# Kernel optimization log

Measured on AMD Instinct MI355X. Metric: run time of the kernel, lower is better.

The kernel has to match this reference:

```python
import jax, jax.numpy as jnp
import numpy as np

C = 64
SHIFT = 3
NEIGHBOR_SIZES = (3, 5, 7)  # dilation = 1 for all levels
NUM_GROUPS = 8


def conv2d(x, w, b, padding=0, groups=1):
    out = jax.lax.conv_general_dilated(
        x, w, (1, 1), [(padding, padding), (padding, padding)],
        dimension_numbers=('NCHW', 'OIHW', 'NCHW'),
        feature_group_count=groups)
    return out + b[None, :, None, None]


def natten_level(q, k, v, rpb, ks):
    # q,k,v: (B,H,W,C) channels-last; rpb: (2ks-1, 2ks-1); dilation=1.
    # NATTEN semantics: window of size ks x ks centered at each query, clamped
    # (shifted) at image borders so it always lies fully inside the image.
    B, H, W, Cc = q.shape
    r = ks // 2
    i = jnp.arange(H); ni = jnp.clip(i - r, 0, H - ks)   # window row starts
    j = jnp.arange(W); nj = jnp.clip(j - r, 0, W - ks)   # window col starts
    ar = jnp.arange(ks)
    ii = ni[:, None] + ar[None, :]                        # (H,ks) neighbor rows
    jj = nj[:, None] + ar[None, :]                        # (W,ks) neighbor cols
    kn = k[:, ii][:, :, :, jj]                            # (B,H,ks,W,ks,C)
    attn = jnp.einsum('bhwc,bhpwqc->bhwpq', q, kn)        # (B,H,W,ks,ks)
    # relative-position-bias lookup: row start pi = (ks-1) + ni - i
    pi = (ks - 1) + ni - i                                # (H,)
    pj = (ks - 1) + nj - j                                # (W,)
    bias = rpb[(pi[:, None] + ar[None, :])[:, None, :, None],
               (pj[:, None] + ar[None, :])[None, :, None, :]]  # (H,W,ks,ks)
    attn = attn + bias[None]
    attn = jax.nn.softmax(attn.reshape(B, H, W, ks * ks), axis=-1)
    attn = attn.reshape(B, H, W, ks, ks)
    vn = v[:, ii][:, :, :, jj]                            # (B,H,ks,W,ks,C)
    return jnp.einsum('bhwpq,bhpwqc->bhwc', attn, vn)


def _forward(sup_frame, key_frame, conv_smooth_w, conv_smooth_b,
             conv_reduce_w, conv_reduce_b, v_w0, v_b0, v_w1, v_b1,
             v_w2, v_b2, rpb0, rpb1, rpb2, fusion_w, fusion_b):
    p = SHIFT
    outs = [sup_frame]  # original (pre-shift) support features
    # shift-roll spatial correlation
    shifts = [(sh, sw) for sh in (-p, 0, p) for sw in (-p, 0, p)
              if not (sh == 0 and sw == 0)]
    padded = jnp.pad(sup_frame, ((0, 0), (0, 0), (p, p), (p, p)))
    parts = jnp.split(padded, NUM_GROUPS, axis=1)
    shifted = jnp.concatenate(
        [jnp.roll(parts[g], shifts[g], axis=(2, 3)) for g in range(NUM_GROUPS)],
        axis=1)[..., p:-p, p:-p]
    shifted = conv2d(shifted, conv_smooth_w, conv_smooth_b, padding=1,
                     groups=NUM_GROUPS)
    sup2 = conv2d(jnp.concatenate([sup_frame, shifted], axis=1),
                  conv_reduce_w, conv_reduce_b)
    # multi-scale neighborhood attention (single head)
    q = jnp.transpose(key_frame, (0, 2, 3, 1))
    k = jnp.transpose(sup2, (0, 2, 3, 1))
    v_ws = (v_w0, v_w1, v_w2); v_bs = (v_b0, v_b1, v_b2)
    rpbs = (rpb0, rpb1, rpb2)
    for lvl, ks in enumerate(NEIGHBOR_SIZES):
        v = jnp.transpose(conv2d(sup2, v_ws[lvl], v_bs[lvl]), (0, 2, 3, 1))
        agg = natten_level(q, k, v, rpbs[lvl], ks)
        outs.append(jnp.transpose(agg, (0, 3, 1, 2)))
    fused = jnp.concatenate(outs, axis=1)  # (B, 4*C, H, W)
    return jax.nn.relu(conv2d(fused, fusion_w, fusion_b, padding=1))


def setup_inputs() -> dict:
    key = jax.random.key(0)
    ks = jax.random.split(key, 20)
    B, H, W = 4, 96, 96
    s = 0.05
    d = {}
    d['sup_frame'] = jax.random.normal(ks[0], (B, C, H, W), jnp.float32)
    d['key_frame'] = jax.random.normal(ks[1], (B, C, H, W), jnp.float32)
    d['conv_smooth_w'] = jax.random.normal(ks[2], (C, C // NUM_GROUPS, 3, 3), jnp.float32) * s
    d['conv_smooth_b'] = jnp.zeros((C,), jnp.float32)
    d['conv_reduce_w'] = jax.random.normal(ks[3], (C, 2 * C, 1, 1), jnp.float32) * s
    d['conv_reduce_b'] = jnp.zeros((C,), jnp.float32)
    for i, nk in enumerate(NEIGHBOR_SIZES):
        d[f'v_w{i}'] = jax.random.normal(ks[4 + i], (C, C, 1, 1), jnp.float32) * s
        d[f'v_b{i}'] = jnp.zeros((C,), jnp.float32)
        d[f'rpb{i}'] = jax.random.normal(ks[8 + i], (2 * nk - 1, 2 * nk - 1), jnp.float32) * 0.02
    d['fusion_w'] = jax.random.normal(ks[12], (C, C * (len(NEIGHBOR_SIZES) + 1), 3, 3), jnp.float32) * s
    d['fusion_b'] = jnp.zeros((C,), jnp.float32)
    return d


def reference(sup_frame, key_frame, conv_smooth_w, conv_smooth_b,
              conv_reduce_w, conv_reduce_b, v_w0, v_b0, v_w1, v_b1,
              v_w2, v_b2, rpb0, rpb1, rpb2, fusion_w, fusion_b):
    return _forward(sup_frame, key_frame, conv_smooth_w, conv_smooth_b,
                    conv_reduce_w, conv_reduce_b, v_w0, v_b0, v_w1, v_b1,
                    v_w2, v_b2, rpb0, rpb1, rpb2, fusion_w, fusion_b)
```

## Files before the change

### kernel.cpp

```cpp
#include <hip/hip_runtime.h>
#include <hip/hip_bf16.h>

#define HW 9216
#define NPX 36864

typedef __attribute__((ext_vector_type(8))) short short8;
typedef __attribute__((ext_vector_type(4))) float f32x4;

static __device__ __forceinline__ unsigned short f2bf(float x) {
    union { __hip_bfloat16 h; unsigned short u; } c; c.h = __float2bfloat16(x); return c.u;
}
static __device__ __forceinline__ float bfl(unsigned int u){ return __uint_as_float(u << 16); }
static __device__ __forceinline__ float bfh(unsigned int u){ return __uint_as_float(u & 0xffff0000u); }

__global__ __launch_bounds__(256) void prep_weights(
    const float* __restrict__ rw, const float* __restrict__ vw0,
    const float* __restrict__ vw1, const float* __restrict__ vw2,
    const float* __restrict__ fw,
    float* __restrict__ rwT, unsigned short* __restrict__ vwF, unsigned short* __restrict__ fwF)
{
    int idx = blockIdx.x * 256 + threadIdx.x;
    if (idx < 8192) {
        int c = idx & 63, i = idx >> 6;
        rwT[idx] = rw[c * 128 + i];
    } else if (idx < 20480) {
        int e = idx - 8192;
        int j = e & 7, lane = (e >> 3) & 63, kf = (e >> 9) & 1, nt = (e >> 10) & 3, lvl = e >> 12;
        int co = nt * 16 + (lane & 15);
        int k = kf * 32 + (lane >> 4) * 8 + j;
        const float* vw = (lvl == 0) ? vw0 : ((lvl == 1) ? vw1 : vw2);
        vwF[e] = f2bf(vw[co * 64 + k]);
    } else if (idx < 167936) {
        int e = idx - 20480;
        int j = e & 7, lane = (e >> 3) & 63, nt = (e >> 9) & 3, kc = e >> 11;
        int co = nt * 16 + (lane & 15);
        int k = kc * 32 + ((lane >> 4) << 3) + j;
        int tap = k >> 8, ci = k & 255;
        fwF[e] = f2bf(fw[co * 2304 + ci * 9 + tap]);
    }
}

__global__ void pack_kernel(const float* __restrict__ key, const float* __restrict__ sup,
                            float* __restrict__ qT, __hip_bfloat16* __restrict__ fused)
{
    __shared__ float lk[32][33], ls[32][33];
    int tx = threadIdx.x, ty = threadIdx.y;
    int x0 = blockIdx.x * 32, c0 = blockIdx.y * 32;
    int z = blockIdx.z; int b = z / 96, y = z - b * 96;
    #pragma unroll
    for (int i = 0; i < 32; i += 8) {
        int c = c0 + ty + i;
        lk[ty + i][tx] = key[((b * 64 + c) * 96 + y) * 96 + x0 + tx];
        ls[ty + i][tx] = sup[((b * 64 + c) * 96 + y) * 96 + x0 + tx];
    }
    __syncthreads();
    #pragma unroll
    for (int i = 0; i < 32; i += 8) {
        int px = (b * 96 + y) * 96 + x0 + ty + i;
        qT[px * 64 + c0 + tx]     = lk[tx][ty + i];
        fused[px * 256 + c0 + tx] = __hip_bfloat16(ls[tx][ty + i]);
    }
}

__global__ __launch_bounds__(256) void shift_smooth(const float* __restrict__ sup,
    const float* __restrict__ w, const float* __restrict__ bias, float* __restrict__ smooth)
{
    __shared__ __align__(16) float tile[8][34][36];
    int bid = blockIdx.x;
    int half = bid & 1;
    int sj   = (bid >> 1) % 9;
    int grp  = (bid / 18) & 7;
    int b    = bid / 144;
    int sby = sj / 3, sbx = sj % 3;
    int Y0 = sby * 32, X0 = sbx * 32;
    int sh = 3 * ((grp >= 5) - (grp < 3));
    int mm = (grp < 3) ? grp : ((grp < 5) ? ((grp == 3) ? 0 : 2) : (grp - 5));
    int sw = 3 * mm - 3;
    int t = threadIdx.x;

    const float* supg = sup + (size_t)(b * 64 + grp * 8) * HW;
    #pragma unroll
    for (int pp = 0; pp < 5; pp++) {
        int pos = pp * 256 + t;
        if (pos < 1156) {
            int r = pos / 34, u = pos - r * 34;
            int yy = Y0 - 1 + r, xx = X0 - 1 + u;
            int ys = yy - sh, xs = xx - sw;
            bool ok = (yy >= 0) & (yy < 96) & (xx >= 0) & (xx < 96) &
                      (ys >= 0) & (ys < 96) & (xs >= 0) & (xs < 96);
            int addr = ok ? (ys * 96 + xs) : 0;
            #pragma unroll
            for (int ic = 0; ic < 8; ic++) {
                float v = supg[(size_t)ic * HW + addr];
                tile[ic][r][u] = ok ? v : 0.f;
            }
        }
    }
    __syncthreads();

    int c = __builtin_amdgcn_readfirstlane(grp * 8 + half * 4 + (t >> 6));
    int lane = t & 63;
    int ty4 = lane >> 3, tx4 = lane & 7;
    int py0 = ty4 * 4, x0r = tx4 * 4;

    float bz = bias[c];
    float acc[4][4];
    #pragma unroll
    for (int jr = 0; jr < 4; jr++)
        #pragma unroll
        for (int j = 0; j < 4; j++) acc[jr][j] = bz;

    const float* wp = w + c * 72;
    for (int ic = 0; ic < 8; ic++) {
        float wr[9];
        #pragma unroll
        for (int q = 0; q < 9; q++) wr[q] = wp[ic * 9 + q];
        #pragma unroll
        for (int rr = 0; rr < 6; rr++) {
            float4 fa = *(const float4*)&tile[ic][py0 + rr][x0r];
            float4 fb4 = *(const float4*)&tile[ic][py0 + rr][x0r + 4];
            float f[6] = {fa.x, fa.y, fa.z, fa.w, fb4.x, fb4.y};
            #pragma unroll
            for (int ky = 0; ky < 3; ky++) {
                int jr = rr - ky;
                if (jr >= 0 && jr < 4) {
                    #pragma unroll
                    for (int j = 0; j < 4; j++)
                        acc[jr][j] += wr[ky*3]*f[j] + wr[ky*3+1]*f[j+1] + wr[ky*3+2]*f[j+2];
                }
            }
        }
    }

    float* op = smooth + ((size_t)(b * 64 + c) * 96 + Y0 + py0) * 96 + X0 + x0r;
    #pragma unroll
    for (int jr = 0; jr < 4; jr++) {
        float4 st = {acc[jr][0], acc[jr][1], acc[jr][2], acc[jr][3]};
        *(float4*)(op + (size_t)jr * 96) = st;
    }
}

__global__ __launch_bounds__(256) void reduce_kernel(const float* __restrict__ sup,
    const float* __restrict__ smooth, const float* __restrict__ rwT,
    const float* __restrict__ rb, float* __restrict__ sup2)
{
    __shared__ __align__(16) float wlds[8192];
    int t = threadIdx.x;
    #pragma unroll
    for (int e = 0; e < 8; e++) {
        int idx = (e * 256 + t) * 4;
        *(float4*)&wlds[idx] = *(const float4*)&rwT[idx];
    }
    __syncthreads();

    int lane = t & 63, wq = t >> 6;
    int px = blockIdx.x * 64 + lane;
    int b = px / HW; int rem = px - b * HW;
    const float* s1 = sup + (size_t)b * 64 * HW + rem;
    const float* s2 = smooth + (size_t)b * 64 * HW + rem;
    float acc[16];
    #pragma unroll
    for (int j = 0; j < 16; j++) acc[j] = rb[wq * 16 + j];

    #pragma unroll 8
    for (int i = 0; i < 64; i++) {
        float v = s1[i * HW];
        const float* wr = &wlds[i * 64 + wq * 16];
        float4 w0 = *(const float4*)wr, w1 = *(const float4*)(wr + 4);
        float4 w2 = *(const float4*)(wr + 8), w3 = *(const float4*)(wr + 12);
        acc[0] += w0.x * v;  acc[1] += w0.y * v;  acc[2] += w0.z * v;  acc[3] += w0.w * v;
        acc[4] += w1.x * v;  acc[5] += w1.y * v;  acc[6] += w1.z * v;  acc[7] += w1.w * v;
        acc[8] += w2.x * v;  acc[9] += w2.y * v;  acc[10] += w2.z * v; acc[11] += w2.w * v;
        acc[12] += w3.x * v; acc[13] += w3.y * v; acc[14] += w3.z * v; acc[15] += w3.w * v;
    }
    #pragma unroll 8
    for (int i = 0; i < 64; i++) {
        float v = s2[i * HW];
        const float* wr = &wlds[(64 + i) * 64 + wq * 16];
        float4 w0 = *(const float4*)wr, w1 = *(const float4*)(wr + 4);
        float4 w2 = *(const float4*)(wr + 8), w3 = *(const float4*)(wr + 12);
        acc[0] += w0.x * v;  acc[1] += w0.y * v;  acc[2] += w0.z * v;  acc[3] += w0.w * v;
        acc[4] += w1.x * v;  acc[5] += w1.y * v;  acc[6] += w1.z * v;  acc[7] += w1.w * v;
        acc[8] += w2.x * v;  acc[9] += w2.y * v;  acc[10] += w2.z * v; acc[11] += w2.w * v;
        acc[12] += w3.x * v; acc[13] += w3.y * v; acc[14] += w3.z * v; acc[15] += w3.w * v;
    }

    float* op = sup2 + (size_t)px * 64 + wq * 16;
    #pragma unroll
    for (int j = 0; j < 16; j += 4) { float4 st = {acc[j], acc[j+1], acc[j+2], acc[j+3]}; *(float4*)(op + j) = st; }
}

template<int KS>
__device__ __forceinline__ void level_softmax(int qc, int y, int x, int ni7, int nj7,
        const _Float16* rpbl, const _Float16* dots_row, _Float16* out_row)
{
    constexpr int R = KS / 2, KK = KS * KS, NB = 2 * KS - 1;
    constexpr int NE = (KK + 7) / 8;
    int ni = min(max(y - R, 0), 96 - KS), nj = min(max(x - R, 0), 96 - KS);
    int di = ni - ni7, dj = nj - nj7;
    int br = KS - 1 + ni - y, bc = KS - 1 + nj - x;
    float sv[NE];
    float mx = -1e30f;
    #pragma unroll
    for (int i = 0; i < NE; i++) {
        int e = qc + i * 8;
        if (e < KK) {
            int ey = e / KS, ex = e - ey * KS;
            float s = (float)dots_row[(di + ey) * 7 + dj + ex] + (float)rpbl[(br + ey) * NB + bc + ex];
            sv[i] = s; mx = fmaxf(mx, s);
        } else sv[i] = -1e30f;
    }
    mx = fmaxf(mx, __shfl_xor(mx, 8)); mx = fmaxf(mx, __shfl_xor(mx, 16)); mx = fmaxf(mx, __shfl_xor(mx, 32));
    float sum = 0.f;
    #pragma unroll
    for (int i = 0; i < NE; i++) { sv[i] = __expf(sv[i] - mx); sum += sv[i]; }
    sum += __shfl_xor(sum, 8); sum += __shfl_xor(sum, 16); sum += __shfl_xor(sum, 32);
    float inv = 1.f / sum;
    #pragma unroll
    for (int i = 0; i < NE; i++) {
        int e = qc + i * 8;
        if (e < KK) out_row[e] = (_Float16)(sv[i] * inv);
    }
}

__global__ __launch_bounds__(256) void natten_fused(
    const float* __restrict__ qT, const float* __restrict__ sup2,
    const unsigned short* __restrict__ vwF,
    const float* __restrict__ vb0, const float* __restrict__ vb1, const float* __restrict__ vb2,
    const float* __restrict__ rpb0, const float* __restrict__ rpb1, const float* __restrict__ rpb2,
    __hip_bfloat16* __restrict__ fused)
{
    __shared__ __align__(16) unsigned short khalo[140 * 72];
    __shared__ _Float16 dots[32][52];
    __shared__ _Float16 a3[32][12];
    __shared__ _Float16 a5[32][28];
    __shared__ _Float16 rlds[276];

    int t = threadIdx.x;
    int bb = blockIdx.y;
    int tx0 = (blockIdx.x % 12) * 8, ty0 = (blockIdx.x / 12) * 4;
    const float* kb = sup2 + (size_t)bb * HW * 64;

    for (int e = t; e < 275; e += 256) {
        float v = (e < 169) ? rpb2[e] : ((e < 250) ? rpb1[e - 169] : rpb0[e - 250]);
        rlds[e] = (_Float16)v;
    }

    for (int it = 0; it < 9; it++) {
        int qidx = it * 256 + t;
        if (qidx < 2240) {
            int cq = qidx & 15, pos = qidx >> 4;
            int py = pos / 14, pxx = pos - py * 14;
            int gy = min(max(ty0 - 3 + py, 0), 95);
            int gx = min(max(tx0 - 3 + pxx, 0), 95);
            float4 v = *(const float4*)(kb + (((size_t)gy * 96 + gx) << 6) + cq * 4);
            ushort4 pk = {f2bf(v.x), f2bf(v.y), f2bf(v.z), f2bf(v.w)};
            *(ushort4*)&khalo[pos * 72 + cq * 4] = pk;
        }
    }
    __syncthreads();

    int lane = t & 63, wv = t >> 6;
    int pxl = wv * 8 + (lane & 7);
    int qc = lane >> 3;
    int pty = pxl >> 3, ptx = pxl & 7;
    int y = ty0 + pty, x = tx0 + ptx;
    int gpx = bb * HW + y * 96 + x;

    float qv[8];
    {
        const float* qp = qT + (size_t)gpx * 64 + qc * 8;
        float4 q0 = *(const float4*)qp, q1 = *(const float4*)(qp + 4);
        qv[0] = q0.x; qv[1] = q0.y; qv[2] = q0.z; qv[3] = q0.w;
        qv[4] = q1.x; qv[5] = q1.y; qv[6] = q1.z; qv[7] = q1.w;
    }

    int ni7 = min(max(y - 3, 0), 89), nj7 = min(max(x - 3, 0), 89);
    int ly = ni7 - (ty0 - 3), lx = nj7 - (tx0 - 3);

    #pragma unroll 1
    for (int oy = 0; oy < 7; oy++) {
        #pragma unroll
        for (int ox = 0; ox < 7; ox++) {
            const unsigned short* kp = &khalo[((ly + oy) * 14 + lx + ox) * 72 + qc * 8];
            uint4 ka = *(const uint4*)kp;
            float p0 = qv[0]*bfl(ka.x) + qv[1]*bfh(ka.x) + qv[2]*bfl(ka.y) + qv[3]*bfh(ka.y);
            float p1 = qv[4]*bfl(ka.z) + qv[5]*bfh(ka.z) + qv[6]*bfl(ka.w) + qv[7]*bfh(ka.w);
            float d = p0 + p1;
            d += __shfl_xor(d, 8);
            d += __shfl_xor(d, 16);
            d += __shfl_xor(d, 32);
            if (qc == 0) dots[pxl][oy * 7 + ox] = (_Float16)d;
        }
    }

    level_softmax<3>(qc, y, x, ni7, nj7, rlds + 250, &dots[pxl][0], &a3[pxl][0]);
    level_softmax<5>(qc, y, x, ni7, nj7, rlds + 169, &dots[pxl][0], &a5[pxl][0]);
    level_softmax<7>(qc, y, x, ni7, nj7, rlds,       &dots[pxl][0], &dots[pxl][0]);

    int ni5 = min(max(y - 2, 0), 91), nj5 = min(max(x - 2, 0), 91);
    int ni3 = min(max(y - 1, 0), 93), nj3 = min(max(x - 1, 0), 93);
    int di5 = ni5 - ni7, dj5 = nj5 - nj7, di3 = ni3 - ni7, dj3 = nj3 - nj7;

    float s2[3][8];
    #pragma unroll
    for (int l = 0; l < 3; l++)
        #pragma unroll
        for (int j = 0; j < 8; j++) s2[l][j] = 0.f;

    #pragma unroll 1
    for (int oy = 0; oy < 7; oy++) {
        #pragma unroll
        for (int ox = 0; ox < 7; ox++) {
            const unsigned short* kp = &khalo[((ly + oy) * 14 + lx + ox) * 72 + qc * 8];
            uint4 ka = *(const uint4*)kp;
            float kv[8] = {bfl(ka.x), bfh(ka.x), bfl(ka.y), bfh(ka.y),
                           bfl(ka.z), bfh(ka.z), bfl(ka.w), bfh(ka.w)};
            float w7 = (float)dots[pxl][oy * 7 + ox];
            #pragma unroll
            for (int j = 0; j < 8; j++) s2[2][j] += w7 * kv[j];
            int e5y = oy - di5, e5x = ox - dj5;
            if ((unsigned)e5y < 5u && (unsigned)e5x < 5u) {
                float w5 = (float)a5[pxl][e5y * 5 + e5x];
                #pragma unroll
                for (int j = 0; j < 8; j++) s2[1][j] += w5 * kv[j];
            }
            int e3y = oy - di3, e3x = ox - dj3;
            if ((unsigned)e3y < 3u && (unsigned)e3x < 3u) {
                float w3 = (float)a3[pxl][e3y * 3 + e3x];
                #pragma unroll
                for (int j = 0; j < 8; j++) s2[0][j] += w3 * kv[j];
            }
        }
    }
    __syncthreads();

    unsigned short* sproj = khalo;
    #pragma unroll
    for (int l = 0; l < 3; l++) {
        unsigned int pk[4];
        #pragma unroll
        for (int j = 0; j < 4; j++)
            pk[j] = (unsigned int)f2bf(s2[l][2*j]) | ((unsigned int)f2bf(s2[l][2*j+1]) << 16);
        uint4 sv = {pk[0], pk[1], pk[2], pk[3]};
        *(uint4*)&sproj[(l * 32 + pxl) * 72 + qc * 8] = sv;
    }
    __syncthreads();

    if (wv < 3) {
        int l = wv;
        int lm = lane & 15, quad = lane >> 4;
        const float* vbl = (l == 0) ? vb0 : ((l == 1) ? vb1 : vb2);
        #pragma unroll
        for (int mt = 0; mt < 2; mt++) {
            f32x4 acc[4];
            #pragma unroll
            for (int nt = 0; nt < 4; nt++) acc[nt] = (f32x4){0.f, 0.f, 0.f, 0.f};
            #pragma unroll
            for (int kf = 0; kf < 2; kf++) {
                short8 a = *(const short8*)&sproj[(l * 32 + mt * 16 + lm) * 72 + kf * 32 + quad * 8];
                #pragma unroll
                for (int nt = 0; nt < 4; nt++) {
                    short8 bfr = *(const short8*)&vwF[(((l * 4 + nt) * 2 + kf) * 64 + lane) * 8];
                    acc[nt] = __builtin_amdgcn_mfma_f32_16x16x32_bf16(a, bfr, acc[nt], 0, 0, 0);
                }
            }
            #pragma unroll
            for (int nt = 0; nt < 4; nt++)
                #pragma unroll
                for (int r = 0; r < 4; r++) {
                    int p = mt * 16 + quad * 4 + r;
                    int co = nt * 16 + lm;
                    int py = p >> 3, pxx = p & 7;
                    size_t off = ((size_t)(bb * HW + (ty0 + py) * 96 + tx0 + pxx) << 8) + (l + 1) * 64 + co;
                    fused[off] = __hip_bfloat16(acc[nt][r] + vbl[co]);
                }
        }
    }
}

__global__ __launch_bounds__(256) void fusion_mfma(
    const __hip_bfloat16* __restrict__ fB, const unsigned short* __restrict__ fwF,
    const float* __restrict__ fb, float* __restrict__ out)
{
    __shared__ __align__(16) unsigned short ah[108 * 72];
    __shared__ float lds_out[64 * 66];
    int t = threadIdx.x;
    int wv = t >> 6, lane = t & 63, lm = lane & 15, quad = lane >> 4;
    int X0 = blockIdx.x * 16, Y0 = blockIdx.y * 4, b = blockIdx.z;
    const unsigned short* fBu = (const unsigned short*)fB;

    f32x4 acc[4] = {};

    for (int chunk = 0; chunk < 4; chunk++) {
        __syncthreads();
        #pragma unroll
        for (int ee = 0; ee < 4; ee++) {
            int e = ee * 256 + t;
            if (e < 864) {
                int seg = e & 7, hp = e >> 3;
                int hy = hp / 18, hx = hp - hy * 18;
                int gy = Y0 - 1 + hy, gx = X0 - 1 + hx;
                bool ok = (gy >= 0) & (gy < 96) & (gx >= 0) & (gx < 96);
                short8 v = {};
                if (ok) v = *(const short8*)(fBu + (((size_t)(b * HW + gy * 96 + gx)) << 8) + chunk * 64 + seg * 8);
                *(short8*)&ah[hp * 72 + seg * 8] = v;
            }
        }
        __syncthreads();
        #pragma unroll
        for (int ky = 0; ky < 3; ky++) {
            #pragma unroll
            for (int kx = 0; kx < 3; kx++) {
                #pragma unroll
                for (int kf = 0; kf < 2; kf++) {
                    short8 a = *(const short8*)&ah[((wv + ky) * 18 + lm + kx) * 72 + kf * 32 + quad * 8];
                    int kc = (ky * 3 + kx) * 8 + chunk * 2 + kf;
                    const unsigned short* bp = fwF + ((size_t)(kc * 4) * 64 + lane) * 8;
                    acc[0] = __builtin_amdgcn_mfma_f32_16x16x32_bf16(a, *(const short8*)(bp),        acc[0], 0, 0, 0);
                    acc[1] = __builtin_amdgcn_mfma_f32_16x16x32_bf16(a, *(const short8*)(bp + 512),  acc[1], 0, 0, 0);
                    acc[2] = __builtin_amdgcn_mfma_f32_16x16x32_bf16(a, *(const short8*)(bp + 1024), acc[2], 0, 0, 0);
                    acc[3] = __builtin_amdgcn_mfma_f32_16x16x32_bf16(a, *(const short8*)(bp + 1536), acc[3], 0, 0, 0);
                }
            }
        }
    }

    #pragma unroll
    for (int nt = 0; nt < 4; nt++)
        #pragma unroll
        for (int r = 0; r < 4; r++) {
            int p = wv * 16 + quad * 4 + r;
            int co = nt * 16 + lm;
            lds_out[co * 66 + p] = acc[nt][r];
        }
    __syncthreads();

    int p2 = t & 63, py = p2 >> 4, px2 = p2 & 15;
    float* ob = out + ((size_t)(b * 64) * 96 + Y0 + py) * 96 + X0 + px2;
    #pragma unroll 4
    for (int i = 0; i < 16; i++) {
        int co = (t >> 6) * 16 + i;
        float v = lds_out[co * 66 + p2] + fb[co];
        ob[(size_t)co * HW] = v > 0.f ? v : 0.f;
    }
}

extern "C" void kernel_launch(void* const* d_in, const int* in_sizes, int n_in,
                              void* d_out, int out_size, void* d_ws, size_t ws_size,
                              hipStream_t stream) {
    const float* sup = (const float*)d_in[0];
    const float* key = (const float*)d_in[1];
    const float* smw = (const float*)d_in[2];
    const float* smb = (const float*)d_in[3];
    const float* rw  = (const float*)d_in[4];
    const float* rb  = (const float*)d_in[5];
    const float *vw[3], *vb[3], *rpb[3];
    if (in_sizes[8] == 25) {
        for (int l = 0; l < 3; l++) {
            vw[l]  = (const float*)d_in[6 + 3 * l];
            vb[l]  = (const float*)d_in[7 + 3 * l];
            rpb[l] = (const float*)d_in[8 + 3 * l];
        }
    } else {
        for (int l = 0; l < 3; l++) {
            vw[l]  = (const float*)d_in[6 + 2 * l];
            vb[l]  = (const float*)d_in[7 + 2 * l];
            rpb[l] = (const float*)d_in[12 + l];
        }
    }
    const float* fw = (const float*)d_in[15];
    const float* fb = (const float*)d_in[16];
    float* out = (float*)d_out;

    float* wsf    = (float*)d_ws;
    float* smooth = wsf;
    float* sup2   = wsf + 2359296;
    float* qT     = wsf + 4718592;
    float* rwT    = wsf + 7077888;
    unsigned short* vwF = (unsigned short*)(wsf + 7086080);
    __hip_bfloat16* fusedB = (__hip_bfloat16*)(wsf + 7092224);
    unsigned short* fwF    = (unsigned short*)(wsf + 11810816);

    prep_weights<<<dim3(656), dim3(256), 0, stream>>>(rw, vw[0], vw[1], vw[2], fw, rwT, vwF, fwF);
    pack_kernel<<<dim3(3, 2, 384), dim3(32, 8), 0, stream>>>(key, sup, qT, fusedB);
    shift_smooth<<<dim3(576), dim3(256), 0, stream>>>(sup, smw, smb, smooth);
    reduce_kernel<<<dim3(576), dim3(256), 0, stream>>>(sup, smooth, rwT, rb, sup2);
    natten_fused<<<dim3(288, 4), dim3(256), 0, stream>>>(qT, sup2, vwF,
        vb[0], vb[1], vb[2], rpb[0], rpb[1], rpb[2], fusedB);
    fusion_mfma<<<dim3(6, 24, 4), dim3(256), 0, stream>>>(fusedB, fwF, fb, out);
}
```

Before: 222.7 us.

## Split QK dot products across lanes by neighbor instead of channel

Queries are staged in LDS, and each of the 8 lanes per pixel now computes whole 64-channel dot products for a subset of the 49 neighbors instead of partial sums over 8 channels. This removes the three cross-lane shuffle reductions per neighbor and the single-lane writes to the dots array. In exchange it adds more LDS traffic, a block-wide barrier, and more registers per lane, which may reduce occupancy.

```diff
diff --git a/kernel.cpp b/kernel.cpp
--- a/kernel.cpp
+++ b/kernel.cpp
@@ -231,6 +231,7 @@
     __hip_bfloat16* __restrict__ fused)
 {
     __shared__ __align__(16) unsigned short khalo[140 * 72];
+    __shared__ __align__(16) float qlds[32][68];
     __shared__ _Float16 dots[32][52];
     __shared__ _Float16 a3[32][12];
     __shared__ _Float16 a5[32][28];
@@ -258,6 +259,12 @@
             *(ushort4*)&khalo[pos * 72 + cq * 4] = pk;
         }
     }
+    #pragma unroll
+    for (int e = t; e < 512; e += 256) {
+        int px = e >> 4, seg = e & 15;
+        float4 v = *(const float4*)(qT + ((size_t)(bb * HW + (ty0 + (px >> 3)) * 96 + tx0 + (px & 7)) << 6) + seg * 4);
+        *(float4*)&qlds[px][seg * 4] = v;
+    }
     __syncthreads();
 
     int lane = t & 63, wv = t >> 6;
@@ -265,34 +272,43 @@
     int qc = lane >> 3;
     int pty = pxl >> 3, ptx = pxl & 7;
     int y = ty0 + pty, x = tx0 + ptx;
-    int gpx = bb * HW + y * 96 + x;
-
-    float qv[8];
-    {
-        const float* qp = qT + (size_t)gpx * 64 + qc * 8;
-        float4 q0 = *(const float4*)qp, q1 = *(const float4*)(qp + 4);
-        qv[0] = q0.x; qv[1] = q0.y; qv[2] = q0.z; qv[3] = q0.w;
-        qv[4] = q1.x; qv[5] = q1.y; qv[6] = q1.z; qv[7] = q1.w;
-    }
 
     int ni7 = min(max(y - 3, 0), 89), nj7 = min(max(x - 3, 0), 89);
     int ly = ni7 - (ty0 - 3), lx = nj7 - (tx0 - 3);
 
+    float dacc[7];
+    #pragma unroll
+    for (int i = 0; i < 7; i++) dacc[i] = 0.f;
     #pragma unroll 1
-    for (int oy = 0; oy < 7; oy++) {
-        #pragma unroll
-        for (int ox = 0; ox < 7; ox++) {
-            const unsigned short* kp = &khalo[((ly + oy) * 14 + lx + ox) * 72 + qc * 8];
-            uint4 ka = *(const uint4*)kp;
-            float p0 = qv[0]*bfl(ka.x) + qv[1]*bfh(ka.x) + qv[2]*bfl(ka.y) + qv[3]*bfh(ka.y);
-            float p1 = qv[4]*bfl(ka.z) + qv[5]*bfh(ka.z) + qv[6]*bfl(ka.w) + qv[7]*bfh(ka.w);
-            float d = p0 + p1;
-            d += __shfl_xor(d, 8);
-            d += __shfl_xor(d, 16);
-            d += __shfl_xor(d, 32);
-            if (qc == 0) dots[pxl][oy * 7 + ox] = (_Float16)d;
-        }
-    }
+    for (int cc = 0; cc < 4; cc++) {
+        float qreg[16];
+        #pragma unroll
+        for (int j = 0; j < 4; j++) {
+            float4 q4 = *(const float4*)&qlds[pxl][cc * 16 + j * 4];
+            qreg[j*4] = q4.x; qreg[j*4+1] = q4.y; qreg[j*4+2] = q4.z; qreg[j*4+3] = q4.w;
+        }
+        #pragma unroll
+        for (int i = 0; i < 7; i++) {
+            int p = qc + 8 * i;
+            if (p < 49) {
+                int oy = p / 7, ox = p - oy * 7;
+                const unsigned short* kp = &khalo[((ly + oy) * 14 + lx + ox) * 72 + cc * 16];
+                uint4 ka = *(const uint4*)kp;
+                uint4 kc2 = *(const uint4*)(kp + 8);
+                float p0 = qreg[0]*bfl(ka.x) + qreg[1]*bfh(ka.x) + qreg[2]*bfl(ka.y) + qreg[3]*bfh(ka.y)
+                         + qreg[4]*bfl(ka.z) + qreg[5]*bfh(ka.z) + qreg[6]*bfl(ka.w) + qreg[7]*bfh(ka.w);
+                float p1 = qreg[8]*bfl(kc2.x) + qreg[9]*bfh(kc2.x) + qreg[10]*bfl(kc2.y) + qreg[11]*bfh(kc2.y)
+                         + qreg[12]*bfl(kc2.z) + qreg[13]*bfh(kc2.z) + qreg[14]*bfl(kc2.w) + qreg[15]*bfh(kc2.w);
+                dacc[i] += p0 + p1;
+            }
+        }
+    }
+    #pragma unroll
+    for (int i = 0; i < 7; i++) {
+        int p = qc + 8 * i;
+        if (p < 49) dots[pxl][p] = (_Float16)dacc[i];
+    }
+    __syncthreads();
 
     level_softmax<3>(qc, y, x, ni7, nj7, rlds + 250, &dots[pxl][0], &a3[pxl][0]);
     level_softmax<5>(qc, y, x, ni7, nj7, rlds + 169, &dots[pxl][0], &a5[pxl][0]);
```

New measurement: 212.6 us. -4.5%, faster.

## Compute NATTEN QK dots with MFMA over the whole tile halo

Applied to the files above, without the earlier changes.

Replaces the per-pixel scalar QK dot products and their shuffle reductions with bf16 MFMA. Each block multiplies its 32 queries against all 140 halo keys and stores the resulting scores in a 32x148 fp16 LDS table, which the softmax then reads by local halo coordinates. Queries are packed as bf16 instead of fp32, which halves query traffic. The dense product computes many unneeded query-key pairs, about 140 per query against 49 needed, and both the larger LDS footprint and bf16 query rounding may cost occupancy or accuracy.

```diff
diff --git a/kernel.cpp b/kernel.cpp
--- a/kernel.cpp
+++ b/kernel.cpp
@@ -41,7 +41,7 @@
 }
 
 __global__ void pack_kernel(const float* __restrict__ key, const float* __restrict__ sup,
-                            float* __restrict__ qT, __hip_bfloat16* __restrict__ fused)
+                            __hip_bfloat16* __restrict__ qB, __hip_bfloat16* __restrict__ fused)
 {
     __shared__ float lk[32][33], ls[32][33];
     int tx = threadIdx.x, ty = threadIdx.y;
@@ -57,7 +57,7 @@
     #pragma unroll
     for (int i = 0; i < 32; i += 8) {
         int px = (b * 96 + y) * 96 + x0 + ty + i;
-        qT[px * 64 + c0 + tx]     = lk[tx][ty + i];
+        qB[px * 64 + c0 + tx]     = __hip_bfloat16(lk[tx][ty + i]);
         fused[px * 256 + c0 + tx] = __hip_bfloat16(ls[tx][ty + i]);
     }
 }
@@ -191,13 +191,13 @@
 }
 
 template<int KS>
-__device__ __forceinline__ void level_softmax(int qc, int y, int x, int ni7, int nj7,
-        const _Float16* rpbl, const _Float16* dots_row, _Float16* out_row)
+__device__ __forceinline__ void level_softmax(int qc, int y, int x, int ty0, int tx0,
+        const _Float16* rpbl, const _Float16* dots_row, _Float16* out_row, bool inplace)
 {
     constexpr int R = KS / 2, KK = KS * KS, NB = 2 * KS - 1;
     constexpr int NE = (KK + 7) / 8;
     int ni = min(max(y - R, 0), 96 - KS), nj = min(max(x - R, 0), 96 - KS);
-    int di = ni - ni7, dj = nj - nj7;
+    int lyL = ni - (ty0 - 3), lxL = nj - (tx0 - 3);
     int br = KS - 1 + ni - y, bc = KS - 1 + nj - x;
     float sv[NE];
     float mx = -1e30f;
@@ -206,7 +206,7 @@
         int e = qc + i * 8;
         if (e < KK) {
             int ey = e / KS, ex = e - ey * KS;
-            float s = (float)dots_row[(di + ey) * 7 + dj + ex] + (float)rpbl[(br + ey) * NB + bc + ex];
+            float s = (float)dots_row[(lyL + ey) * 14 + lxL + ex] + (float)rpbl[(br + ey) * NB + bc + ex];
             sv[i] = s; mx = fmaxf(mx, s);
         } else sv[i] = -1e30f;
     }
@@ -219,19 +219,25 @@
     #pragma unroll
     for (int i = 0; i < NE; i++) {
         int e = qc + i * 8;
-        if (e < KK) out_row[e] = (_Float16)(sv[i] * inv);
+        if (e < KK) {
+            int ey = e / KS, ex = e - ey * KS;
+            _Float16 wv16 = (_Float16)(sv[i] * inv);
+            if (inplace) ((_Float16*)dots_row)[(lyL + ey) * 14 + lxL + ex] = wv16;
+            else out_row[e] = wv16;
+        }
     }
 }
 
 __global__ __launch_bounds__(256) void natten_fused(
-    const float* __restrict__ qT, const float* __restrict__ sup2,
+    const __hip_bfloat16* __restrict__ qB, const float* __restrict__ sup2,
     const unsigned short* __restrict__ vwF,
     const float* __restrict__ vb0, const float* __restrict__ vb1, const float* __restrict__ vb2,
     const float* __restrict__ rpb0, const float* __restrict__ rpb1, const float* __restrict__ rpb2,
     __hip_bfloat16* __restrict__ fused)
 {
     __shared__ __align__(16) unsigned short khalo[140 * 72];
-    __shared__ _Float16 dots[32][52];
+    __shared__ __align__(16) unsigned short qlds[32 * 72];
+    __shared__ _Float16 dotsF[32][148];
     __shared__ _Float16 a3[32][12];
     __shared__ _Float16 a5[32][28];
     __shared__ _Float16 rlds[276];
@@ -258,45 +264,54 @@
             *(ushort4*)&khalo[pos * 72 + cq * 4] = pk;
         }
     }
+    if (t < 256) {
+        int px = t >> 3, seg = t & 7;
+        short8 v = *(const short8*)((const unsigned short*)qB +
+            ((size_t)(bb * HW + (ty0 + (px >> 3)) * 96 + tx0 + (px & 7)) << 6) + seg * 8);
+        *(short8*)&qlds[px * 72 + seg * 8] = v;
+    }
     __syncthreads();
 
     int lane = t & 63, wv = t >> 6;
+    int lm = lane & 15, quad = lane >> 4;
+
+    #pragma unroll
+    for (int ni = 0; ni < 3; ni++) {
+        int nt = wv + ni * 4;
+        if (nt <= 8) {
+            int hp = nt * 16 + lm;
+            int hpr = min(hp, 139);
+            f32x4 acc0 = {0.f, 0.f, 0.f, 0.f}, acc1 = {0.f, 0.f, 0.f, 0.f};
+            #pragma unroll
+            for (int kt = 0; kt < 2; kt++) {
+                short8 bfrag = *(const short8*)&khalo[hpr * 72 + kt * 32 + quad * 8];
+                short8 a0 = *(const short8*)&qlds[lm * 72 + kt * 32 + quad * 8];
+                short8 a1 = *(const short8*)&qlds[(16 + lm) * 72 + kt * 32 + quad * 8];
+                acc0 = __builtin_amdgcn_mfma_f32_16x16x32_bf16(a0, bfrag, acc0, 0, 0, 0);
+                acc1 = __builtin_amdgcn_mfma_f32_16x16x32_bf16(a1, bfrag, acc1, 0, 0, 0);
+            }
+            if (hp < 140) {
+                #pragma unroll
+                for (int r = 0; r < 4; r++) {
+                    dotsF[quad * 4 + r][hp]      = (_Float16)acc0[r];
+                    dotsF[16 + quad * 4 + r][hp] = (_Float16)acc1[r];
+                }
+            }
+        }
+    }
+    __syncthreads();
+
     int pxl = wv * 8 + (lane & 7);
     int qc = lane >> 3;
     int pty = pxl >> 3, ptx = pxl & 7;
     int y = ty0 + pty, x = tx0 + ptx;
-    int gpx = bb * HW + y * 96 + x;
-
-    float qv[8];
-    {
-        const float* qp = qT + (size_t)gpx * 64 + qc * 8;
-        float4 q0 = *(const float4*)qp, q1 = *(const float4*)(qp + 4);
-        qv[0] = q0.x; qv[1] = q0.y; qv[2] = q0.z; qv[3] = q0.w;
-        qv[4] = q1.x; qv[5] = q1.y; qv[6] = q1.z; qv[7] = q1.w;
-    }
 
     int ni7 = min(max(y - 3, 0), 89), nj7 = min(max(x - 3, 0), 89);
     int ly = ni7 - (ty0 - 3), lx = nj7 - (tx0 - 3);
 
-    #pragma unroll 1
-    for (int oy = 0; oy < 7; oy++) {
-        #pragma unroll
-        for (int ox = 0; ox < 7; ox++) {
-            const unsigned short* kp = &khalo[((ly + oy) * 14 + lx + ox) * 72 + qc * 8];
-            uint4 ka = *(const uint4*)kp;
-            float p0 = qv[0]*bfl(ka.x) + qv[1]*bfh(ka.x) + qv[2]*bfl(ka.y) + qv[3]*bfh(ka.y);
-            float p1 = qv[4]*bfl(ka.z) + qv[5]*bfh(ka.z) + qv[6]*bfl(ka.w) + qv[7]*bfh(ka.w);
-            float d = p0 + p1;
-            d += __shfl_xor(d, 8);
-            d += __shfl_xor(d, 16);
-            d += __shfl_xor(d, 32);
-            if (qc == 0) dots[pxl][oy * 7 + ox] = (_Float16)d;
-        }
-    }
-
-    level_softmax<3>(qc, y, x, ni7, nj7, rlds + 250, &dots[pxl][0], &a3[pxl][0]);
-    level_softmax<5>(qc, y, x, ni7, nj7, rlds + 169, &dots[pxl][0], &a5[pxl][0]);
-    level_softmax<7>(qc, y, x, ni7, nj7, rlds,       &dots[pxl][0], &dots[pxl][0]);
+    level_softmax<3>(qc, y, x, ty0, tx0, rlds + 250, &dotsF[pxl][0], &a3[pxl][0], false);
+    level_softmax<5>(qc, y, x, ty0, tx0, rlds + 169, &dotsF[pxl][0], &a5[pxl][0], false);
+    level_softmax<7>(qc, y, x, ty0, tx0, rlds,       &dotsF[pxl][0], nullptr,     true);
 
     int ni5 = min(max(y - 2, 0), 91), nj5 = min(max(x - 2, 0), 91);
     int ni3 = min(max(y - 1, 0), 93), nj3 = min(max(x - 1, 0), 93);
@@ -316,7 +331,7 @@
             uint4 ka = *(const uint4*)kp;
             float kv[8] = {bfl(ka.x), bfh(ka.x), bfl(ka.y), bfh(ka.y),
                            bfl(ka.z), bfh(ka.z), bfl(ka.w), bfh(ka.w)};
-            float w7 = (float)dots[pxl][oy * 7 + ox];
+            float w7 = (float)dotsF[pxl][(ly + oy) * 14 + lx + ox];
             #pragma unroll
             for (int j = 0; j < 8; j++) s2[2][j] += w7 * kv[j];
             int e5y = oy - di5, e5x = ox - dj5;
@@ -349,7 +364,6 @@
 
     if (wv < 3) {
         int l = wv;
-        int lm = lane & 15, quad = lane >> 4;
         const float* vbl = (l == 0) ? vb0 : ((l == 1) ? vb1 : vb2);
         #pragma unroll
         for (int mt = 0; mt < 2; mt++) {
@@ -476,17 +490,17 @@
     float* wsf    = (float*)d_ws;
     float* smooth = wsf;
     float* sup2   = wsf + 2359296;
-    float* qT     = wsf + 4718592;
+    __hip_bfloat16* qBuf = (__hip_bfloat16*)(wsf + 4718592);
     float* rwT    = wsf + 7077888;
     unsigned short* vwF = (unsigned short*)(wsf + 7086080);
     __hip_bfloat16* fusedB = (__hip_bfloat16*)(wsf + 7092224);
     unsigned short* fwF    = (unsigned short*)(wsf + 11810816);
 
     prep_weights<<<dim3(656), dim3(256), 0, stream>>>(rw, vw[0], vw[1], vw[2], fw, rwT, vwF, fwF);
-    pack_kernel<<<dim3(3, 2, 384), dim3(32, 8), 0, stream>>>(key, sup, qT, fusedB);
+    pack_kernel<<<dim3(3, 2, 384), dim3(32, 8), 0, stream>>>(key, sup, qBuf, fusedB);
     shift_smooth<<<dim3(576), dim3(256), 0, stream>>>(sup, smw, smb, smooth);
     reduce_kernel<<<dim3(576), dim3(256), 0, stream>>>(sup, smooth, rwT, rb, sup2);
-    natten_fused<<<dim3(288, 4), dim3(256), 0, stream>>>(qT, sup2, vwF,
+    natten_fused<<<dim3(288, 4), dim3(256), 0, stream>>>(qBuf, sup2, vwF,
         vb[0], vb[1], vb[2], rpb[0], rpb[1], rpb[2], fusedB);
     fusion_mfma<<<dim3(6, 24, 4), dim3(256), 0, stream>>>(fusedB, fwF, fb, out);
 }
```

Measured after the change: 205.4 us. -7.8%, faster.
